# Kernel optimization log

Measured on AMD Instinct MI355X. Metric: run time of the kernel, lower is better.

Reference implementation:

```python
import jax, jax.numpy as jnp
import numpy as np

N, E, IN, H, D, C = 30000, 400000, 128, 4, 64, 40
EPS = 1e-5
SLOPE = 0.2  # DGL GATv2Conv leaky_relu negative_slope default


def setup_inputs() -> dict:
    key = jax.random.key(0)
    ks = jax.random.split(key, 20)
    def rn(k, shape, s=0.05):
        return jax.random.normal(k, shape, jnp.float32) * s
    return {
        "x": jax.random.normal(ks[0], (N, IN), jnp.float32),
        "src": jax.random.randint(ks[1], (E,), 0, N),
        "dst": jax.random.randint(ks[2], (E,), 0, N),
        # layer 0: in=128 -> heads*64 (residual projection since 128 != 256)
        "W_src0": rn(ks[3], (IN, H * D)), "W_dst0": rn(ks[4], (IN, H * D)),
        "b0": jnp.zeros((H * D,), jnp.float32), "attn0": rn(ks[5], (H, D)),
        "res_W0": rn(ks[6], (IN, H * D)),
        # layer 1: 256 -> heads*64 (identity residual since 256 == 256)
        "W_src1": rn(ks[7], (H * D, H * D)), "W_dst1": rn(ks[8], (H * D, H * D)),
        "b1": jnp.zeros((H * D,), jnp.float32), "attn1": rn(ks[9], (H, D)),
        # layer 2: 256 -> heads*40 (residual projection)
        "W_src2": rn(ks[10], (H * D, H * C)), "W_dst2": rn(ks[11], (H * D, H * C)),
        "b2": jnp.zeros((H * C,), jnp.float32), "attn2": rn(ks[12], (H, C)),
        "res_W2": rn(ks[13], (H * D, H * C)),
        # batchnorm affine params (training-mode batch stats)
        "g0": jnp.ones((H * D,), jnp.float32), "be0": jnp.zeros((H * D,), jnp.float32),
        "g1": jnp.ones((H * D,), jnp.float32), "be1": jnp.zeros((H * D,), jnp.float32),
    }


def gatv2_layer(h, src, dst, Wsrc, Wdst, b, attn, resW, out_dim, relu_act):
    # DGL GATv2Conv: score_e = attn . leaky_relu(fc_src(h)[u] + fc_dst(h)[v])
    n = h.shape[0]
    fs = (h @ Wsrc).reshape(n, H, out_dim)
    fd = (h @ Wdst).reshape(n, H, out_dim)
    e = jax.nn.leaky_relu(fs[src] + fd[dst], SLOPE)      # [E, H, out]
    score = jnp.einsum("ehd,hd->eh", e, attn)            # [E, H]
    # segment softmax over incoming edges of each dst node
    m = jax.ops.segment_max(score, dst, num_segments=n)
    m = jnp.where(jnp.isfinite(m), m, 0.0)               # zero in-degree safety
    ex = jnp.exp(score - m[dst])
    denom = jax.ops.segment_sum(ex, dst, num_segments=n)
    alpha = ex / jnp.maximum(denom, 1e-9)[dst]
    rst = jax.ops.segment_sum(alpha[:, :, None] * fs[src], dst, num_segments=n)
    res = (h @ resW).reshape(n, H, out_dim) if resW is not None else h.reshape(n, H, out_dim)
    rst = rst + res + b.reshape(1, H, out_dim)
    return jax.nn.relu(rst) if relu_act else rst


def batchnorm(h, g, be):
    mu = h.mean(0)
    var = h.var(0)  # biased variance, as torch BN uses for normalization
    return g * (h - mu) * jax.lax.rsqrt(var + EPS) + be


def reference(x, src, dst, W_src0, W_dst0, b0, attn0, res_W0, W_src1, W_dst1, b1, attn1, W_src2, W_dst2, b2, attn2, res_W2, g0, be0, g1, be1):
    h = gatv2_layer(x, src, dst, W_src0, W_dst0, b0, attn0, res_W0, D, True)
    h = jax.nn.relu(batchnorm(h.reshape(N, H * D), g0, be0))  # dropout = identity (eval)
    h = gatv2_layer(h, src, dst, W_src1, W_dst1, b1, attn1, None, D, True)
    h = jax.nn.relu(batchnorm(h.reshape(N, H * D), g1, be1))
    h = gatv2_layer(h, src, dst, W_src2, W_dst2, b2, attn2, res_W2, C, False)
    h = h.mean(1)  # mean over heads -> [N, C]
    return jax.nn.log_softmax(h, axis=-1)
```

## Files before the change

### kernel.cpp

```cpp
#include <hip/hip_runtime.h>
#include <hip/hip_bf16.h>
#include <math.h>

#define NN 30000
#define EE 400000
#define INP 128
#define HH 4
#define DD 64
#define CC 40
#define HD 256
#define HC 160

typedef unsigned short ushort;
typedef __attribute__((ext_vector_type(8))) short s8v;
typedef __attribute__((ext_vector_type(4))) float f4v;


__device__ inline ushort bf16_of_float(float f) {
    __hip_bfloat16 b = __float2bfloat16(f);
    return *(ushort*)&b;
}
__device__ __forceinline__ float2 cvt2(unsigned d) {
    return make_float2(__uint_as_float(d << 16), __uint_as_float(d & 0xFFFF0000u));
}
__device__ __forceinline__ float b2f(ushort u) { return __uint_as_float(((unsigned)u) << 16); }

__device__ __forceinline__ float2 f2add(float2 a, float2 b){ return make_float2(a.x+b.x, a.y+b.y); }
__device__ __forceinline__ float2 f2mul(float2 a, float2 b){ return make_float2(a.x*b.x, a.y*b.y); }
__device__ __forceinline__ float2 f2muls(float2 a, float s){ return make_float2(a.x*s, a.y*s); }
__device__ __forceinline__ float2 f2max(float2 a, float2 b){ return make_float2(fmaxf(a.x,b.x), fmaxf(a.y,b.y)); }
__device__ __forceinline__ float2 f2fma(float2 a, float2 b, float2 c){
    return make_float2(__fmaf_rn(a.x,b.x,c.x), __fmaf_rn(a.y,b.y,c.y));
}

__device__ __forceinline__ void gld16(const void* g, void* l) {
    __builtin_amdgcn_global_load_lds((const __attribute__((address_space(1))) void*)g,
                                     (__attribute__((address_space(3))) void*)l, 16, 0, 0);
}

__device__ __forceinline__ float rowsum16(float x) {
    int t;
    t = __builtin_amdgcn_update_dpp(0, __float_as_int(x), 0x128, 0xF, 0xF, false); x += __int_as_float(t);
    t = __builtin_amdgcn_update_dpp(0, __float_as_int(x), 0x124, 0xF, 0xF, false); x += __int_as_float(t);
    t = __builtin_amdgcn_update_dpp(0, __float_as_int(x), 0x122, 0xF, 0xF, false); x += __int_as_float(t);
    t = __builtin_amdgcn_update_dpp(0, __float_as_int(x), 0x121, 0xF, 0xF, false); x += __int_as_float(t);
    return x;
}
__device__ __forceinline__ float rowmax16(float x) {
    int t;
    t = __builtin_amdgcn_update_dpp(0, __float_as_int(x), 0x128, 0xF, 0xF, false); x = fmaxf(x, __int_as_float(t));
    t = __builtin_amdgcn_update_dpp(0, __float_as_int(x), 0x124, 0xF, 0xF, false); x = fmaxf(x, __int_as_float(t));
    t = __builtin_amdgcn_update_dpp(0, __float_as_int(x), 0x122, 0xF, 0xF, false); x = fmaxf(x, __int_as_float(t));
    t = __builtin_amdgcn_update_dpp(0, __float_as_int(x), 0x121, 0xF, 0xF, false); x = fmaxf(x, __int_as_float(t));
    return x;
}

#define XB 3750
#define TB 1408
#define ZB 240

__global__ __launch_bounds__(256) void k_prep(const float* __restrict__ x, ushort* __restrict__ xc,
        const float* W0, const float* W1, const float* W2, const float* W3,
        const float* W4, const float* W5, const float* W6, const float* W7,
        ushort* bt0, ushort* bt1, ushort* bt2,
        int* __restrict__ zero_region,
        const float* b0, const float* a0, const float* b1, const float* a1,
        const float* b2, const float* a2, const float* g0, const float* be0,
        const float* g1, const float* be1, ushort* __restrict__ smallv) {
    int b = blockIdx.x, t = threadIdx.x;
    if (b < XB) {
        int i = b * 256 + t;
        if (i < NN * INP / 4) {
            float4 v = ((const float4*)x)[i];
            ushort4 o;
            o.x = bf16_of_float(v.x); o.y = bf16_of_float(v.y);
            o.z = bf16_of_float(v.z); o.w = bf16_of_float(v.w);
            ((ushort4*)xc)[i] = o;
        }
    } else if (b < XB + TB) {
        const float* Ws[8] = {W0, W1, W2, W3, W4, W5, W6, W7};
        int g = (b - XB) * 256 + t;
        if (g < 98304) {
            int seg = g >> 15, local = g & 32767;
            int n = local >> 7, k = local & 127;
            bt0[g] = bf16_of_float(Ws[seg][k * 256 + n]);
        } else if (g < 229376) {
            int gg = g - 98304;
            int seg = gg >> 16, local = gg & 65535;
            int n = local >> 8, k = local & 255;
            bt1[gg] = bf16_of_float(Ws[3 + seg][k * 256 + n]);
        } else if (g < 360448) {
            int gg = g - 229376;
            int n = gg >> 8, k = gg & 255;
            ushort val = 0;
            if (n < 480) {
                int seg = n / 160;
                int nn = n - seg * 160;
                val = bf16_of_float(Ws[5 + seg][k * 160 + nn]);
            }
            bt2[gg] = val;
        }
    } else if (b < XB + TB + ZB) {
        int i = (b - XB - TB) * 256 + t;
        if (i < 1024 + 2 * NN + 192) zero_region[i] = 0;
    } else {
        const float* ptrs[10] = {b0, a0, b1, a1, b2, a2, g0, be0, g1, be1};
        const int sz[10] = {256, 256, 256, 256, 160, 160, 256, 256, 256, 256};
        int off = 0;
        for (int j = 0; j < 10; j++) {
            if (t < sz[j]) smallv[off + t] = bf16_of_float(ptrs[j][t]);
            off += sz[j];
        }
    }
}


__global__ __launch_bounds__(256) void k_hist(const int* __restrict__ dst, int* __restrict__ cnt) {
    int e = blockIdx.x * 256 + threadIdx.x;
    if (e < EE) atomicAdd(&cnt[dst[e]], 1);
}

__global__ __launch_bounds__(256) void k_binhist(const int* __restrict__ cnt, int* __restrict__ binCnt) {
    __shared__ int lb[64];
    int t = threadIdx.x;
    if (t < 64) lb[t] = 0;
    __syncthreads();
    int i = blockIdx.x * 256 + t;
    if (i < NN) atomicAdd(&lb[63 - min(cnt[i], 63)], 1);
    __syncthreads();
    if (t < 64 && lb[t] > 0) atomicAdd(&binCnt[t], lb[t]);
}

__global__ __launch_bounds__(256) void k_beg(const int* __restrict__ cnt, int* __restrict__ beg,
                                             int* __restrict__ total) {
    __shared__ int ss[256];
    __shared__ int base;
    int t = threadIdx.x;
    int i = blockIdx.x * 256 + t;
    int c = (i < NN) ? cnt[i] : 0;
    ss[t] = c;
    __syncthreads();
    for (int o = 1; o < 256; o <<= 1) {
        int v = (t >= o) ? ss[t - o] : 0;
        __syncthreads();
        ss[t] += v;
        __syncthreads();
    }
    if (t == 255) base = atomicAdd(total, ss[255]);
    __syncthreads();
    if (i < NN) beg[i] = base + ss[t] - c;
}

__global__ __launch_bounds__(256) void k_order(const int* __restrict__ cnt, const int* __restrict__ binCnt,
                                               int* __restrict__ binPos, int* __restrict__ order) {
    __shared__ int lb[64], lbase[64], bpre[64];
    int t = threadIdx.x;
    if (t < 64) { lb[t] = 0; bpre[t] = binCnt[t]; }
    __syncthreads();
    int i = blockIdx.x * 256 + t;
    int bin = 0, rank = 0;
    if (i < NN) {
        bin = 63 - min(cnt[i], 63);
        rank = atomicAdd(&lb[bin], 1);
    }
    for (int o = 1; o < 64; o <<= 1) {
        int v = (t >= o && t < 64) ? bpre[t - o] : 0;
        __syncthreads();
        if (t < 64) bpre[t] += v;
        __syncthreads();
    }
    if (t < 64 && lb[t] > 0)
        lbase[t] = bpre[t] - binCnt[t] + atomicAdd(&binPos[t], lb[t]);
    __syncthreads();
    if (i < NN) order[lbase[bin] + rank] = i;
}

__global__ __launch_bounds__(256) void k_scatter(const int* __restrict__ src, const int* __restrict__ dst,
                                                 const int* __restrict__ beg, int* __restrict__ pos,
                                                 int* __restrict__ srcs) {
    int e = blockIdx.x * 256 + threadIdx.x;
    if (e < EE) {
        int d = dst[e];
        int p = atomicAdd(&pos[d], 1);
        srcs[beg[d] + p] = src[e];
    }
}


template<int K, int SEGW, int NSEG>
__global__ __launch_bounds__(256) void k_gemm_tiled(const ushort* __restrict__ A,
                                                    const ushort* __restrict__ Bt,
                                                    ushort* __restrict__ o0, ushort* __restrict__ o1,
                                                    ushort* __restrict__ o2) {
    __shared__ ushort As[128 * 32];
    __shared__ ushort Bs[128 * 32];
    int t = threadIdx.x;
    int wave = t >> 6, lane = t & 63;
    int m = lane & 15, q = lane >> 4;
    int row0 = blockIdx.x * 128, col0 = blockIdx.y * 128;
    int wr = (wave >> 1) << 6, wc = (wave & 1) << 6;
    f4v acc[4][4] = {};
    int c1 = t, c2 = t + 256;
    int ar1 = min(row0 + (c1 >> 2), NN - 1);
    int ar2 = min(row0 + (c2 >> 2), NN - 1);
    const ushort* a1 = A + (size_t)ar1 * K + (c1 & 3) * 8;
    const ushort* a2 = A + (size_t)ar2 * K + (c2 & 3) * 8;
    const ushort* b1 = Bt + (size_t)(col0 + (c1 >> 2)) * K + (c1 & 3) * 8;
    const ushort* b2 = Bt + (size_t)(col0 + (c2 >> 2)) * K + (c2 & 3) * 8;
    int wbase = wave << 10;
    char* AsB = (char*)As;
    char* BsB = (char*)Bs;

#pragma unroll
    for (int kt = 0; kt < K; kt += 32) {
        __syncthreads();
        gld16(a1 + kt, AsB + wbase);
        gld16(a2 + kt, AsB + 4096 + wbase);
        gld16(b1 + kt, BsB + wbase);
        gld16(b2 + kt, BsB + 4096 + wbase);
        __syncthreads();
        s8v af[4], bg[4];
#pragma unroll
        for (int i = 0; i < 4; i++) af[i] = *(const s8v*)&As[(wr + i * 16 + m) * 32 + q * 8];
#pragma unroll
        for (int c = 0; c < 4; c++) bg[c] = *(const s8v*)&Bs[(wc + c * 16 + m) * 32 + q * 8];
#pragma unroll
        for (int i = 0; i < 4; i++)
#pragma unroll
            for (int c = 0; c < 4; c++)
                acc[i][c] = __builtin_amdgcn_mfma_f32_16x16x32_bf16(bg[c], af[i], acc[i][c], 0, 0, 0);
    }

#pragma unroll
    for (int c = 0; c < 4; c++) {
        int gcb = col0 + wc + c * 16;
        if (gcb < SEGW * NSEG) {
            int seg = gcb / SEGW;
            int colb = gcb - seg * SEGW + q * 4;
            ushort* op = seg == 0 ? o0 : (seg == 1 ? o1 : o2);
#pragma unroll
            for (int i = 0; i < 4; i++) {
                int gr = row0 + wr + i * 16 + m;
                if (gr < NN) {
                    ushort4 s4;
                    s4.x = bf16_of_float(acc[i][c][0]);
                    s4.y = bf16_of_float(acc[i][c][1]);
                    s4.z = bf16_of_float(acc[i][c][2]);
                    s4.w = bf16_of_float(acc[i][c][3]);
                    *(ushort4*)&op[(size_t)gr * SEGW + colb] = s4;
                }
            }
        }
    }
}


template<int DH, bool FINAL>
__global__ __launch_bounds__(256) void k_aggregate(const ushort* __restrict__ fs, const ushort* __restrict__ fd,
                                                   const ushort* __restrict__ res,
                                                   const ushort* __restrict__ attn,
                                                   const ushort* __restrict__ bias,
                                                   const int* __restrict__ beg, const int* __restrict__ cnt,
                                                   const int* __restrict__ srcs,
                                                   const int* __restrict__ order,
                                                   ushort* __restrict__ outb, float* __restrict__ outf) {
    constexpr int F = HH * DH;
    constexpr int JMAX = DH >> 2;
    int tt = threadIdx.x;
    int v = __builtin_amdgcn_readfirstlane(order[blockIdx.x * 4 + (tt >> 6)]);
    int lane = tt & 63;
    int h = lane >> 4, j = lane & 15;
    bool act = j < JMAX;
    unsigned off = h * DH + 4 * j;
    unsigned vbase = (unsigned)v * F + off;
    float2 fda = {0.f,0.f}, fdb = {0.f,0.f}, ava = {0.f,0.f}, avb = {0.f,0.f};
    if (act) {
        uint2 d = *(const uint2*)&fd[vbase];
        fda = cvt2(d.x); fdb = cvt2(d.y);
        uint2 a = *(const uint2*)&attn[off];
        const float LOG2E = 1.4426950408889634f;
        ava = f2muls(cvt2(a.x), LOG2E); avb = f2muls(cvt2(a.y), LOG2E);
    }
    float l = 0.f;
    float2 acca = {0.f,0.f}, accb = {0.f,0.f};
    int b0i = beg[v], end = b0i + cnt[v];

    auto ldrow = [&](int u, float2& ra, float2& rb) {
        ra = make_float2(0.f, 0.f); rb = make_float2(0.f, 0.f);
        if (act) {
            uint2 d = *(const uint2*)&fs[(unsigned)u * F + off];
            ra = cvt2(d.x); rb = cvt2(d.y);
        }
    };
    auto dotlr = [&](const float2& ra, const float2& rb) -> float {
        float2 t0 = f2add(ra, fda);
        float2 t1 = f2add(rb, fdb);
        t0 = f2max(t0, f2muls(t0, 0.2f));
        t1 = f2max(t1, f2muls(t1, 0.2f));
        float2 p2 = f2mul(ava, t0);
        p2 = f2fma(avb, t1, p2);
        return p2.x + p2.y;
    };

    int i = b0i;
    for (; i + 3 < end; i += 4) {
        int u0 = srcs[i], u1 = srcs[i+1], u2 = srcs[i+2], u3 = srcs[i+3];
        float2 r0a, r0b, r1a, r1b, r2a, r2b, r3a, r3b;
        ldrow(u0, r0a, r0b); ldrow(u1, r1a, r1b);
        ldrow(u2, r2a, r2b); ldrow(u3, r3a, r3b);
        float p0 = rowsum16(dotlr(r0a, r0b));
        float p1 = rowsum16(dotlr(r1a, r1b));
        float p2 = rowsum16(dotlr(r2a, r2b));
        float p3 = rowsum16(dotlr(r3a, r3b));
        float w0 = exp2f(p0), w1 = exp2f(p1), w2 = exp2f(p2), w3 = exp2f(p3);
        l += (w0 + w1) + (w2 + w3);
        acca = f2fma(make_float2(w0, w0), r0a, acca);
        accb = f2fma(make_float2(w0, w0), r0b, accb);
        acca = f2fma(make_float2(w1, w1), r1a, acca);
        accb = f2fma(make_float2(w1, w1), r1b, accb);
        acca = f2fma(make_float2(w2, w2), r2a, acca);
        accb = f2fma(make_float2(w2, w2), r2b, accb);
        acca = f2fma(make_float2(w3, w3), r3a, acca);
        accb = f2fma(make_float2(w3, w3), r3b, accb);
    }
    for (; i < end; i++) {
        float2 ra, rb;
        ldrow(srcs[i], ra, rb);
        float p0 = rowsum16(dotlr(ra, rb));
        float w0 = exp2f(p0);
        l += w0;
        acca = f2fma(make_float2(w0, w0), ra, acca);
        accb = f2fma(make_float2(w0, w0), rb, accb);
    }

    float4 o4 = {0.f, 0.f, 0.f, 0.f};
    if (act) {
        float inv = 1.f / fmaxf(l, 1e-9f);
        uint2 rr = *(const uint2*)&res[vbase];
        float2 rl = cvt2(rr.x), rh = cvt2(rr.y);
        uint2 bb = *(const uint2*)&bias[off];
        float2 bl = cvt2(bb.x), bh = cvt2(bb.y);
        o4.x = acca.x * inv + rl.x + bl.x;
        o4.y = acca.y * inv + rl.y + bl.y;
        o4.z = accb.x * inv + rh.x + bh.x;
        o4.w = accb.y * inv + rh.y + bh.y;
        if (!FINAL) {
            o4.x = fmaxf(o4.x, 0.f); o4.y = fmaxf(o4.y, 0.f);
            o4.z = fmaxf(o4.z, 0.f); o4.w = fmaxf(o4.w, 0.f);
        }
    }
    if (!FINAL) {
        if (act) {
            ushort4 s4;
            s4.x = bf16_of_float(o4.x); s4.y = bf16_of_float(o4.y);
            s4.z = bf16_of_float(o4.z); s4.w = bf16_of_float(o4.w);
            *(ushort4*)&outb[vbase] = s4;
        }
    } else {
#pragma unroll
        for (int msk = 16; msk <= 32; msk <<= 1) {
            o4.x += __shfl_xor(o4.x, msk, 64);
            o4.y += __shfl_xor(o4.y, msk, 64);
            o4.z += __shfl_xor(o4.z, msk, 64);
            o4.w += __shfl_xor(o4.w, msk, 64);
        }
        float4 zv = make_float4(0.25f * o4.x, 0.25f * o4.y, 0.25f * o4.z, 0.25f * o4.w);
        float mx4 = act ? fmaxf(fmaxf(zv.x, zv.y), fmaxf(zv.z, zv.w)) : -1e30f;
        float mx = rowmax16(mx4);
        float es = 0.f;
        if (act) es = __expf(zv.x - mx) + __expf(zv.y - mx) + __expf(zv.z - mx) + __expf(zv.w - mx);
        float ssum = rowsum16(es);
        float lse = mx + logf(ssum);
        if (act && h == 0) {
            float4 w4 = make_float4(zv.x - lse, zv.y - lse, zv.z - lse, zv.w - lse);
            *(float4*)&outf[(size_t)v * CC + 4 * j] = w4;
        }
    }
}


__global__ __launch_bounds__(256) void k_bn_partial(const ushort* __restrict__ h, float* __restrict__ sum,
                                                    float* __restrict__ sumsq) {
    int c = threadIdx.x;
    int r0 = blockIdx.x * 128;
    int r1 = min(NN, r0 + 128);
    float s = 0.f, ss = 0.f;
    for (int r = r0; r < r1; r++) {
        float vv = b2f(h[(size_t)r * HD + c]);
        s += vv; ss += vv * vv;
    }
    atomicAdd(&sum[c], s);
    atomicAdd(&sumsq[c], ss);
}


__global__ __launch_bounds__(256) void k_bn_norm(const ushort* __restrict__ hin, const float* __restrict__ sum,
                                                 const float* __restrict__ sumsq,
                                                 const ushort* __restrict__ g,
                                                 const ushort* __restrict__ be,
                                                 ushort* __restrict__ hbf) {
    int i4 = blockIdx.x * 256 + threadIdx.x;
    if (i4 < NN * HD / 4) {
        int base = i4 * 4;
        int c = base & (HD - 1);
        ushort4 hv = ((const ushort4*)hin)[i4];
        ushort4 ov;
        float vv[4] = {b2f(hv.x), b2f(hv.y), b2f(hv.z), b2f(hv.w)};
        ushort* po = (ushort*)&ov;
#pragma unroll
        for (int k = 0; k < 4; k++) {
            float mean = sum[c + k] * (1.0f / NN);
            float var = fmaxf(sumsq[c + k] * (1.0f / NN) - mean * mean, 0.f);
            float y = b2f(g[c + k]) * (vv[k] - mean) * rsqrtf(var + 1e-5f) + b2f(be[c + k]);
            po[k] = bf16_of_float(fmaxf(y, 0.f));
        }
        ((ushort4*)hbf)[i4] = ov;
    }
}


static inline char* alignup(char* p) { return (char*)(((size_t)p + 255) & ~(size_t)255); }

extern "C" void kernel_launch(void* const* d_in, const int* in_sizes, int n_in,
                              void* d_out, int out_size, void* d_ws, size_t ws_size,
                              hipStream_t stream) {
    const float* x     = (const float*)d_in[0];
    const int*  src    = (const int*)d_in[1];
    const int*  dst    = (const int*)d_in[2];
    const float* Wsrc0 = (const float*)d_in[3];
    const float* Wdst0 = (const float*)d_in[4];
    const float* b0    = (const float*)d_in[5];
    const float* attn0 = (const float*)d_in[6];
    const float* resW0 = (const float*)d_in[7];
    const float* Wsrc1 = (const float*)d_in[8];
    const float* Wdst1 = (const float*)d_in[9];
    const float* b1    = (const float*)d_in[10];
    const float* attn1 = (const float*)d_in[11];
    const float* Wsrc2 = (const float*)d_in[12];
    const float* Wdst2 = (const float*)d_in[13];
    const float* b2    = (const float*)d_in[14];
    const float* attn2 = (const float*)d_in[15];
    const float* resW2 = (const float*)d_in[16];
    const float* g0    = (const float*)d_in[17];
    const float* be0   = (const float*)d_in[18];
    const float* g1    = (const float*)d_in[19];
    const float* be1   = (const float*)d_in[20];

    char* w = (char*)d_ws;
    const size_t NF = (size_t)NN * HD;
    ushort* fsb = (ushort*)w; w += NF * 2;
    ushort* fdb = (ushort*)w; w += NF * 2;
    ushort* resb= (ushort*)w; w += NF * 2;
    ushort* hag = (ushort*)w; w += NF * 2;
    ushort* hbf = (ushort*)w; w += NF * 2;
    ushort* xc  = (ushort*)w; w += (size_t)NN * INP * 2;
    ushort* bt0 = (ushort*)w; w += 768 * 128 * 2;
    ushort* bt1 = (ushort*)w; w += 512 * 256 * 2;
    ushort* bt2 = (ushort*)w; w += 512 * 256 * 2;
    ushort* smallv = (ushort*)w; w += 2368 * 2; w = alignup(w);
    float* bnstats = (float*)w; w += 1024 * 4;
    int* cnt    = (int*)w; w += NN * 4;
    int* pos    = (int*)w; w += NN * 4;
    int* binCnt = (int*)w; w += 64 * 4;
    int* binPos = (int*)w; w += 64 * 4;
    int* total  = (int*)w; w += 64 * 4; w = alignup(w);
    int* beg    = (int*)w; w += NN * 4; w = alignup(w);
    int* order  = (int*)w; w += NN * 4; w = alignup(w);
    int* srcs   = (int*)w; w += EE * 4;

    const ushort* c_b0    = smallv + 0;
    const ushort* c_attn0 = smallv + 256;
    const ushort* c_b1    = smallv + 512;
    const ushort* c_attn1 = smallv + 768;
    const ushort* c_b2    = smallv + 1024;
    const ushort* c_attn2 = smallv + 1184;
    const ushort* c_g0    = smallv + 1344;
    const ushort* c_be0   = smallv + 1600;
    const ushort* c_g1    = smallv + 1856;
    const ushort* c_be1   = smallv + 2112;

    k_prep<<<XB + TB + ZB + 1, 256, 0, stream>>>(x, xc,
        Wsrc0, Wdst0, resW0, Wsrc1, Wdst1, Wsrc2, Wdst2, resW2, bt0, bt1, bt2,
        (int*)bnstats,
        b0, attn0, b1, attn1, b2, attn2, g0, be0, g1, be1, smallv);

    const int NB = (NN + 255) / 256;
    k_hist<<<(EE + 255) / 256, 256, 0, stream>>>(dst, cnt);
    k_binhist<<<NB, 256, 0, stream>>>(cnt, binCnt);
    k_beg<<<NB, 256, 0, stream>>>(cnt, beg, total);
    k_order<<<NB, 256, 0, stream>>>(cnt, binCnt, binPos, order);
    k_scatter<<<(EE + 255) / 256, 256, 0, stream>>>(src, dst, beg, pos, srcs);

    const int MB = (NN + 127) / 128;

    k_gemm_tiled<128, 256, 3><<<dim3(MB, 6), 256, 0, stream>>>(xc, bt0, fsb, fdb, resb);
    k_aggregate<DD, false><<<NN / 4, 256, 0, stream>>>(fsb, fdb, resb, c_attn0, c_b0,
        beg, cnt, srcs, order, hag, nullptr);
    k_bn_partial<<<MB, 256, 0, stream>>>(hag, bnstats, bnstats + 256);
    k_bn_norm<<<(int)((NF / 4 + 255) / 256), 256, 0, stream>>>(hag, bnstats, bnstats + 256,
                                                               c_g0, c_be0, hbf);

    k_gemm_tiled<256, 256, 2><<<dim3(MB, 4), 256, 0, stream>>>(hbf, bt1, fsb, fdb, nullptr);
    k_aggregate<DD, false><<<NN / 4, 256, 0, stream>>>(fsb, fdb, hbf, c_attn1, c_b1,
        beg, cnt, srcs, order, hag, nullptr);
    k_bn_partial<<<MB, 256, 0, stream>>>(hag, bnstats + 512, bnstats + 768);
    k_bn_norm<<<(int)((NF / 4 + 255) / 256), 256, 0, stream>>>(hag, bnstats + 512, bnstats + 768,
                                                               c_g1, c_be1, hbf);

    k_gemm_tiled<256, 160, 3><<<dim3(MB, 4), 256, 0, stream>>>(hbf, bt2, fsb, fdb, resb);
    k_aggregate<CC, true><<<NN / 4, 256, 0, stream>>>(fsb, fdb, resb, c_attn2, c_b2,
        beg, cnt, srcs, order, nullptr, (float*)d_out);
}
```

Baseline: 409.4 us.

## Fuse graph-preprocessing kernels, software-pipeline aggregate gathers, unroll BN partial sums

Merges the bin-histogram and prefix-scan kernels into one, and the order and edge-scatter kernels into one launch split by block index. This cuts the preprocessing chain from five launches to three. The aggregation loop now double-buffers its row gathers, issuing the next four neighbour loads before computing on the current four, to hide gather latency at the cost of more registers. The BatchNorm partial-sum loop is unrolled with two independent accumulators.

```diff
diff --git a/kernel.cpp b/kernel.cpp
--- a/kernel.cpp
+++ b/kernel.cpp
@@ -10,6 +10,7 @@
 #define CC 40
 #define HD 256
 #define HC 160
+#define NBLK 118
 
 typedef unsigned short ushort;
 typedef __attribute__((ext_vector_type(8))) short s8v;
@@ -120,26 +121,20 @@
     if (e < EE) atomicAdd(&cnt[dst[e]], 1);
 }
 
-__global__ __launch_bounds__(256) void k_binhist(const int* __restrict__ cnt, int* __restrict__ binCnt) {
+__global__ __launch_bounds__(256) void k_binbeg(const int* __restrict__ cnt, int* __restrict__ binCnt,
+                                                int* __restrict__ beg, int* __restrict__ total) {
     __shared__ int lb[64];
+    __shared__ int ss[256];
+    __shared__ int base;
     int t = threadIdx.x;
     if (t < 64) lb[t] = 0;
     __syncthreads();
     int i = blockIdx.x * 256 + t;
-    if (i < NN) atomicAdd(&lb[63 - min(cnt[i], 63)], 1);
+    int c = (i < NN) ? cnt[i] : 0;
+    if (i < NN) atomicAdd(&lb[63 - min(c, 63)], 1);
+    ss[t] = c;
     __syncthreads();
     if (t < 64 && lb[t] > 0) atomicAdd(&binCnt[t], lb[t]);
-}
-
-__global__ __launch_bounds__(256) void k_beg(const int* __restrict__ cnt, int* __restrict__ beg,
-                                             int* __restrict__ total) {
-    __shared__ int ss[256];
-    __shared__ int base;
-    int t = threadIdx.x;
-    int i = blockIdx.x * 256 + t;
-    int c = (i < NN) ? cnt[i] : 0;
-    ss[t] = c;
-    __syncthreads();
     for (int o = 1; o < 256; o <<= 1) {
         int v = (t >= o) ? ss[t - o] : 0;
         __syncthreads();
@@ -151,38 +146,39 @@
     if (i < NN) beg[i] = base + ss[t] - c;
 }
 
-__global__ __launch_bounds__(256) void k_order(const int* __restrict__ cnt, const int* __restrict__ binCnt,
-                                               int* __restrict__ binPos, int* __restrict__ order) {
-    __shared__ int lb[64], lbase[64], bpre[64];
+__global__ __launch_bounds__(256) void k_orderscatter(const int* __restrict__ cnt, const int* __restrict__ binCnt,
+                                                      int* __restrict__ binPos, int* __restrict__ order,
+                                                      const int* __restrict__ src, const int* __restrict__ dst,
+                                                      const int* __restrict__ beg, int* __restrict__ pos,
+                                                      int* __restrict__ srcs) {
     int t = threadIdx.x;
-    if (t < 64) { lb[t] = 0; bpre[t] = binCnt[t]; }
-    __syncthreads();
-    int i = blockIdx.x * 256 + t;
-    int bin = 0, rank = 0;
-    if (i < NN) {
-        bin = 63 - min(cnt[i], 63);
-        rank = atomicAdd(&lb[bin], 1);
-    }
-    for (int o = 1; o < 64; o <<= 1) {
-        int v = (t >= o && t < 64) ? bpre[t - o] : 0;
+    if (blockIdx.x < NBLK) {
+        __shared__ int lb[64], lbase[64], bpre[64];
+        if (t < 64) { lb[t] = 0; bpre[t] = binCnt[t]; }
         __syncthreads();
-        if (t < 64) bpre[t] += v;
+        int i = blockIdx.x * 256 + t;
+        int bin = 0, rank = 0;
+        if (i < NN) {
+            bin = 63 - min(cnt[i], 63);
+            rank = atomicAdd(&lb[bin], 1);
+        }
+        for (int o = 1; o < 64; o <<= 1) {
+            int v = (t >= o && t < 64) ? bpre[t - o] : 0;
+            __syncthreads();
+            if (t < 64) bpre[t] += v;
+            __syncthreads();
+        }
+        if (t < 64 && lb[t] > 0)
+            lbase[t] = bpre[t] - binCnt[t] + atomicAdd(&binPos[t], lb[t]);
         __syncthreads();
-    }
-    if (t < 64 && lb[t] > 0)
-        lbase[t] = bpre[t] - binCnt[t] + atomicAdd(&binPos[t], lb[t]);
-    __syncthreads();
-    if (i < NN) order[lbase[bin] + rank] = i;
-}
-
-__global__ __launch_bounds__(256) void k_scatter(const int* __restrict__ src, const int* __restrict__ dst,
-                                                 const int* __restrict__ beg, int* __restrict__ pos,
-                                                 int* __restrict__ srcs) {
-    int e = blockIdx.x * 256 + threadIdx.x;
-    if (e < EE) {
-        int d = dst[e];
-        int p = atomicAdd(&pos[d], 1);
-        srcs[beg[d] + p] = src[e];
+        if (i < NN) order[lbase[bin] + rank] = i;
+    } else {
+        int e = (blockIdx.x - NBLK) * 256 + t;
+        if (e < EE) {
+            int d = dst[e];
+            int p = atomicAdd(&pos[d], 1);
+            srcs[beg[d] + p] = src[e];
+        }
     }
 }
 
@@ -301,13 +297,8 @@
         p2 = f2fma(avb, t1, p2);
         return p2.x + p2.y;
     };
-
-    int i = b0i;
-    for (; i + 3 < end; i += 4) {
-        int u0 = srcs[i], u1 = srcs[i+1], u2 = srcs[i+2], u3 = srcs[i+3];
-        float2 r0a, r0b, r1a, r1b, r2a, r2b, r3a, r3b;
-        ldrow(u0, r0a, r0b); ldrow(u1, r1a, r1b);
-        ldrow(u2, r2a, r2b); ldrow(u3, r3a, r3b);
+    auto quadc = [&](const float2& r0a, const float2& r0b, const float2& r1a, const float2& r1b,
+                     const float2& r2a, const float2& r2b, const float2& r3a, const float2& r3b) {
         float p0 = rowsum16(dotlr(r0a, r0b));
         float p1 = rowsum16(dotlr(r1a, r1b));
         float p2 = rowsum16(dotlr(r2a, r2b));
@@ -322,6 +313,24 @@
         accb = f2fma(make_float2(w2, w2), r2b, accb);
         acca = f2fma(make_float2(w3, w3), r3a, acca);
         accb = f2fma(make_float2(w3, w3), r3b, accb);
+    };
+
+    int i = b0i;
+    if (i + 3 < end) {
+        int u0 = srcs[i], u1 = srcs[i+1], u2 = srcs[i+2], u3 = srcs[i+3];
+        float2 r0a, r0b, r1a, r1b, r2a, r2b, r3a, r3b;
+        ldrow(u0, r0a, r0b); ldrow(u1, r1a, r1b);
+        ldrow(u2, r2a, r2b); ldrow(u3, r3a, r3b);
+        for (i += 4; i + 3 < end; i += 4) {
+            int n0 = srcs[i], n1 = srcs[i+1], n2 = srcs[i+2], n3 = srcs[i+3];
+            float2 s0a, s0b, s1a, s1b, s2a, s2b, s3a, s3b;
+            ldrow(n0, s0a, s0b); ldrow(n1, s1a, s1b);
+            ldrow(n2, s2a, s2b); ldrow(n3, s3a, s3b);
+            quadc(r0a, r0b, r1a, r1b, r2a, r2b, r3a, r3b);
+            r0a = s0a; r0b = s0b; r1a = s1a; r1b = s1b;
+            r2a = s2a; r2b = s2b; r3a = s3a; r3b = s3b;
+        }
+        quadc(r0a, r0b, r1a, r1b, r2a, r2b, r3a, r3b);
     }
     for (; i < end; i++) {
         float2 ra, rb;
@@ -384,13 +393,21 @@
     int c = threadIdx.x;
     int r0 = blockIdx.x * 128;
     int r1 = min(NN, r0 + 128);
-    float s = 0.f, ss = 0.f;
-    for (int r = r0; r < r1; r++) {
-        float vv = b2f(h[(size_t)r * HD + c]);
-        s += vv; ss += vv * vv;
-    }
-    atomicAdd(&sum[c], s);
-    atomicAdd(&sumsq[c], ss);
+    float s0 = 0.f, ss0 = 0.f, s1 = 0.f, ss1 = 0.f;
+    int r = r0;
+#pragma unroll 4
+    for (; r + 1 < r1; r += 2) {
+        float v0 = b2f(h[(size_t)r * HD + c]);
+        float v1 = b2f(h[(size_t)(r + 1) * HD + c]);
+        s0 += v0; ss0 = __fmaf_rn(v0, v0, ss0);
+        s1 += v1; ss1 = __fmaf_rn(v1, v1, ss1);
+    }
+    if (r < r1) {
+        float v0 = b2f(h[(size_t)r * HD + c]);
+        s0 += v0; ss0 = __fmaf_rn(v0, v0, ss0);
+    }
+    atomicAdd(&sum[c], s0 + s1);
+    atomicAdd(&sumsq[c], ss0 + ss1);
 }
 
 
@@ -484,12 +501,10 @@
         (int*)bnstats,
         b0, attn0, b1, attn1, b2, attn2, g0, be0, g1, be1, smallv);
 
-    const int NB = (NN + 255) / 256;
     k_hist<<<(EE + 255) / 256, 256, 0, stream>>>(dst, cnt);
-    k_binhist<<<NB, 256, 0, stream>>>(cnt, binCnt);
-    k_beg<<<NB, 256, 0, stream>>>(cnt, beg, total);
-    k_order<<<NB, 256, 0, stream>>>(cnt, binCnt, binPos, order);
-    k_scatter<<<(EE + 255) / 256, 256, 0, stream>>>(src, dst, beg, pos, srcs);
+    k_binbeg<<<NBLK, 256, 0, stream>>>(cnt, binCnt, beg, total);
+    k_orderscatter<<<NBLK + (EE + 255) / 256, 256, 0, stream>>>(cnt, binCnt, binPos, order,
+                                                                src, dst, beg, pos, srcs);
 
     const int MB = (NN + 127) / 128;
 
```

Result: faster. 358.7 us (-12.4%).
